# Kernel optimization log

Measured on AMD Instinct MI355X. Metric: run time of the kernel, lower is better.

Reference implementation:

```python
import jax, jax.numpy as jnp
import numpy as np

N, E, F_IN, F_E, G = 40000, 640000, 64, 16, 1000
H = F_IN * 4          # 256, GeneralConv out
O = 128               # GATv2 out (heads=1)
NEG_SLOPE = 0.2


def _glorot(key, shape):
    fan_in, fan_out = shape[0], shape[-1]
    s = jnp.sqrt(6.0 / (fan_in + fan_out))
    return jax.random.uniform(key, shape, jnp.float32, -s, s)


def setup_inputs() -> dict:
    key = jax.random.key(0)
    ks = jax.random.split(key, 20)
    x = jax.random.normal(ks[0], (N, F_IN), jnp.float32)
    edge_index = jax.random.randint(ks[1], (2, E), 0, N, jnp.int64)
    edge_attr = jax.random.normal(ks[2], (E, F_E), jnp.float32)
    batch = jnp.sort(jax.random.randint(ks[3], (N,), 0, G, jnp.int64))
    return {
        "x": x, "edge_index": edge_index, "edge_attr": edge_attr, "batch": batch,
        # GeneralConv params
        "W_msg": _glorot(ks[4], (F_IN, H)), "b_msg": jnp.zeros((H,), jnp.float32),
        "W_edge1": _glorot(ks[5], (F_E, H)), "b_edge1": jnp.zeros((H,), jnp.float32),
        "W_self": _glorot(ks[6], (F_IN, H)), "b_self": jnp.zeros((H,), jnp.float32),
        # GATv2 params (heads=1)
        "W_l": _glorot(ks[7], (H, O)), "b_l": jnp.zeros((O,), jnp.float32),
        "W_r": _glorot(ks[8], (H, O)), "b_r": jnp.zeros((O,), jnp.float32),
        "W_e2": _glorot(ks[9], (F_E, O)),
        "att": _glorot(ks[10], (O, 1))[:, 0],
        "bias2": jnp.zeros((O,), jnp.float32),
        # FFN
        "W1": _glorot(ks[11], (O, 4 * O)), "b1": jnp.zeros((4 * O,), jnp.float32),
        "W2": _glorot(ks[12], (4 * O, 1)), "b2": jnp.zeros((1,), jnp.float32),
    }


def _forward(x, edge_attr, W_msg, b_msg, W_edge1, b_edge1, W_self, b_self,
             W_l, b_l, W_r, b_r, W_e2, att, bias2, W1, b1, W2, b2,
             edge_index, batch):
    src, dst = edge_index[0], edge_index[1]
    # --- GeneralConv: msg = lin_msg(x_j) + lin_edge(edge_attr), sum-aggr at dst, + lin_self(x)
    msg = (x[src] @ W_msg + b_msg) + (edge_attr @ W_edge1 + b_edge1)  # [E,H]
    h = jax.ops.segment_sum(msg, dst, num_segments=N) + (x @ W_self + b_self)
    h = jax.nn.gelu(h, approximate=True)
    # --- GATv2Conv with self-loops (fill_value='mean' for self-loop edge_attr)
    deg = jax.ops.segment_sum(jnp.ones((E,), jnp.float32), dst, num_segments=N)
    loop_attr = jax.ops.segment_sum(edge_attr, dst, num_segments=N) / jnp.maximum(deg, 1.0)[:, None]
    nodes = jnp.arange(N, dtype=src.dtype)
    s = jnp.concatenate([src, nodes])            # [E+N]
    d = jnp.concatenate([dst, nodes])
    ea = jnp.concatenate([edge_attr, loop_attr], axis=0)
    xl = h @ W_l + b_l                           # source transform [N,O]
    xr = h @ W_r + b_r                           # target transform [N,O]
    m = xl[s] + xr[d] + ea @ W_e2                # [E+N,O]
    m = jax.nn.leaky_relu(m, NEG_SLOPE)
    alpha = m @ att                              # [E+N]
    amax = jax.ops.segment_max(alpha, d, num_segments=N)
    ea_exp = jnp.exp(alpha - amax[d])
    denom = jax.ops.segment_sum(ea_exp, d, num_segments=N)
    alpha = ea_exp / denom[d]
    out = jax.ops.segment_sum(xl[s] * alpha[:, None], d, num_segments=N) + bias2  # [N,O]
    # --- global mean pool by graph id
    cnt = jax.ops.segment_sum(jnp.ones((N,), jnp.float32), batch, num_segments=G)
    g = jax.ops.segment_sum(out, batch, num_segments=G) / jnp.maximum(cnt, 1.0)[:, None]
    # --- FFN
    y = jax.nn.gelu(g @ W1 + b1, approximate=True) @ W2 + b2  # [G,1]
    return y


def reference(x, edge_index, edge_attr, batch, W_msg, b_msg, W_edge1, b_edge1,
              W_self, b_self, W_l, b_l, W_r, b_r, W_e2, att, bias2,
              W1, b1, W2, b2):
    return _forward(x, edge_attr, W_msg, b_msg, W_edge1, b_edge1, W_self, b_self,
                    W_l, b_l, W_r, b_r, W_e2, att, bias2, W1, b1, W2, b2,
                    edge_index, batch)
```

## Files before the change

kernel.cpp:

```cpp
#include <hip/hip_runtime.h>
#include <hip/hip_bf16.h>

#define NN 40000
#define NE 640000
#define NG 1000

typedef __attribute__((ext_vector_type(8))) short short8;
typedef __attribute__((ext_vector_type(4))) float f32x4;
typedef __attribute__((ext_vector_type(2))) __bf16 bf16x2v;

__device__ __forceinline__ float gelu_t(float x) {
    float u = 0.7978845608028654f * (x + 0.044715f * x * x * x);
    return 0.5f * x * (1.0f + tanhf(u));
}
__device__ __forceinline__ void atomAddF(float* p, float v) {
    unsafeAtomicAdd(p, v);
}
__device__ __forceinline__ int rfl(int v) { return __builtin_amdgcn_readfirstlane(v); }
__device__ __forceinline__ unsigned short f2bf(float f) {
    unsigned u = __float_as_uint(f);
    unsigned r = (u + 0x7fffu + ((u >> 16) & 1u)) >> 16;
    return (unsigned short)r;
}
__device__ __forceinline__ unsigned pk_bf(float lo, float hi) {
    __hip_bfloat162 v = __float22bfloat162_rn(make_float2(lo, hi));
    unsigned r;
    __builtin_memcpy(&r, &v, 4);
    return r;
}
__device__ __forceinline__ float bfl(unsigned p) { return __uint_as_float(p << 16); }
__device__ __forceinline__ float bfh(unsigned p) { return __uint_as_float(p & 0xffff0000u); }

__device__ __forceinline__ float dot2bf(unsigned a, unsigned b, float c) {
#if __has_builtin(__builtin_amdgcn_fdot2_f32_bf16)
    bf16x2v av, bv;
    __builtin_memcpy(&av, &a, 4);
    __builtin_memcpy(&bv, &b, 4);
    return __builtin_amdgcn_fdot2_f32_bf16(av, bv, c, false);
#else
    return c + bfl(a) * bfl(b) + bfh(a) * bfh(b);
#endif
}

__global__ __launch_bounds__(256) void k_pre(
    const float* __restrict__ x, const int* __restrict__ dst,
    const float* __restrict__ W_self, const float* __restrict__ W_msg,
    const float* __restrict__ W_e1, const float* __restrict__ b_msg,
    const float* __restrict__ b_e1,
    const float* __restrict__ W_l, const float* __restrict__ W_r,
    const float* __restrict__ W_e2,
    unsigned short* __restrict__ x_bf, int* __restrict__ hist,
    int* __restrict__ rank,
    unsigned short* __restrict__ wf1, unsigned short* __restrict__ wf2,
    unsigned* __restrict__ we2p, float* __restrict__ bsum2) {
    int t = blockIdx.x * 256 + threadIdx.x;
    float4 v = ((const float4*)x)[t];
    ((uint2*)x_bf)[t] = make_uint2(pk_bf(v.x, v.y), pk_bf(v.z, v.w));
    rank[t] = atomicAdd(&hist[dst[t]], 1);
    if (t < 256) bsum2[t] = b_msg[t] + b_e1[t];
    if (t < 5120) {
        int l = t & 63;
        int kt = (t >> 6) % 5;
        int gnt = t / 320;
        int n = gnt * 16 + (l & 15);
        int k0 = kt * 32 + (l >> 4) * 8;
        unsigned short vv[8];
        #pragma unroll
        for (int j = 0; j < 8; ++j) {
            int k = k0 + j;
            float wv;
            if (k < 64)       wv = W_self[(size_t)k * 256 + n];
            else if (k < 128) wv = W_msg[(size_t)(k - 64) * 256 + n];
            else if (k < 144) wv = W_e1[(size_t)(k - 128) * 256 + n];
            else              wv = 0.f;
            vv[j] = f2bf(wv);
        }
        uint4 pack;
        pack.x = (unsigned)vv[0] | ((unsigned)vv[1] << 16);
        pack.y = (unsigned)vv[2] | ((unsigned)vv[3] << 16);
        pack.z = (unsigned)vv[4] | ((unsigned)vv[5] << 16);
        pack.w = (unsigned)vv[6] | ((unsigned)vv[7] << 16);
        ((uint4*)wf1)[t] = pack;
    }
    if (t >= 5120 && t < 13312) {
        int t2 = t - 5120;
        int l = t2 & 63;
        int kt = (t2 >> 6) & 7;
        int gnt = t2 >> 9;
        int n = gnt * 16 + (l & 15);
        int k0 = kt * 32 + (l >> 4) * 8;
        const float* W = (n < 128) ? W_l : W_r;
        int nn = n & 127;
        float w[8];
        #pragma unroll
        for (int j = 0; j < 8; ++j) w[j] = W[(size_t)(k0 + j) * 128 + nn];
        uint4 pack;
        pack.x = pk_bf(w[0], w[1]);
        pack.y = pk_bf(w[2], w[3]);
        pack.z = pk_bf(w[4], w[5]);
        pack.w = pk_bf(w[6], w[7]);
        ((uint4*)wf2)[t2] = pack;
    }
    if (t >= 13312 && t < 14336) {
        int t3 = t - 13312;
        int tt = t3 >> 7;
        int c = t3 & 127;
        we2p[t3] = pk_bf(W_e2[(size_t)(2 * tt) * 128 + c],
                         W_e2[(size_t)(2 * tt + 1) * 128 + c]);
    }
}

__global__ __launch_bounds__(1024) void k_scan(const int* __restrict__ hist,
                                               int* __restrict__ row_ptr) {
    __shared__ int ssum[1024];
    int t = threadIdx.x;
    int base = t * 40;
    int local[40];
    int s = 0;
    #pragma unroll
    for (int j = 0; j < 40; ++j) {
        int idx = base + j;
        int v = (idx < NN) ? hist[idx] : 0;
        local[j] = s;
        s += v;
    }
    ssum[t] = s;
    __syncthreads();
    for (int off = 1; off < 1024; off <<= 1) {
        int tmp = (t >= off) ? ssum[t - off] : 0;
        __syncthreads();
        ssum[t] += tmp;
        __syncthreads();
    }
    int prefix = (t > 0) ? ssum[t - 1] : 0;
    #pragma unroll
    for (int j = 0; j < 40; ++j) {
        int idx = base + j;
        if (idx < NN) row_ptr[idx] = prefix + local[j];
    }
    if (t == 0) row_ptr[NN] = NE;
}

__global__ __launch_bounds__(256) void k_scatter(const int* __restrict__ src,
                                                 const int* __restrict__ dst,
                                                 const int* __restrict__ rank,
                                                 const int* __restrict__ row_ptr,
                                                 const float* __restrict__ eattr,
                                                 int* __restrict__ csr_src,
                                                 unsigned short* __restrict__ ea_csr) {
    int e = blockIdx.x * 256 + threadIdx.x;
    if (e >= NE) return;
    int d = dst[e];
    int pos = row_ptr[d] + rank[e];
    csr_src[pos] = src[e];
    const float4* ep = (const float4*)(eattr + (size_t)e * 16);
    float4 a = ep[0], b = ep[1], c = ep[2], dd = ep[3];
    uint4 q0, q1;
    q0.x = pk_bf(a.x, a.y); q0.y = pk_bf(a.z, a.w);
    q0.z = pk_bf(b.x, b.y); q0.w = pk_bf(b.z, b.w);
    q1.x = pk_bf(c.x, c.y); q1.y = pk_bf(c.z, c.w);
    q1.z = pk_bf(dd.x, dd.y); q1.w = pk_bf(dd.z, dd.w);
    uint4* out = (uint4*)ea_csr;
    out[(size_t)pos * 2]     = q0;
    out[(size_t)pos * 2 + 1] = q1;
}

__global__ __launch_bounds__(256) void k_agg(
    const unsigned short* __restrict__ x_bf, const unsigned short* __restrict__ ea_csr,
    const int* __restrict__ csr_src, const int* __restrict__ row_ptr,
    unsigned short* __restrict__ aggx_bf, unsigned short* __restrict__ aggea_bf,
    float* __restrict__ degf) {
    int d = rfl(blockIdx.x * 4 + (threadIdx.x >> 6));
    int lane = threadIdx.x & 63;
    if (d >= NN) return;
    int beg = row_ptr[d], end = row_ptr[d + 1];
    const unsigned* xw = (const unsigned*)x_bf;
    const unsigned* eaw = (const unsigned*)ea_csr;
    int h = lane >> 5;
    int c2 = lane & 31;
    float sxa0 = 0.f, sxa1 = 0.f, sxb0 = 0.f, sxb1 = 0.f;
    int i = beg + h;
    for (; i + 2 < end; i += 4) {
        int sA = csr_src[i];
        int sB = csr_src[i + 2];
        unsigned wA = xw[(size_t)sA * 32 + c2];
        unsigned wB = xw[(size_t)sB * 32 + c2];
        sxa0 += bfl(wA); sxa1 += bfh(wA);
        sxb0 += bfl(wB); sxb1 += bfh(wB);
    }
    if (i < end) {
        int s = csr_src[i];
        unsigned w = xw[(size_t)s * 32 + c2];
        sxa0 += bfl(w); sxa1 += bfh(w);
    }
    float sx0 = sxa0 + sxb0, sx1 = sxa1 + sxb1;
    sx0 += __shfl_xor(sx0, 32, 64);
    sx1 += __shfl_xor(sx1, 32, 64);
    float se0 = 0.f, se1 = 0.f, se0b = 0.f, se1b = 0.f;
    int p = beg * 8 + lane;
    int pend = end * 8;
    for (; p + 64 < pend; p += 128) {
        unsigned w = eaw[p];
        unsigned w2 = eaw[p + 64];
        se0 += bfl(w); se1 += bfh(w);
        se0b += bfl(w2); se1b += bfh(w2);
    }
    if (p < pend) {
        unsigned w = eaw[p];
        se0 += bfl(w); se1 += bfh(w);
    }
    se0 += se0b; se1 += se1b;
    #pragma unroll
    for (int off = 8; off < 64; off <<= 1) {
        se0 += __shfl_xor(se0, off, 64);
        se1 += __shfl_xor(se1, off, 64);
    }
    if (h == 0) ((unsigned*)aggx_bf)[(size_t)d * 32 + c2] = pk_bf(sx0, sx1);
    if (lane < 8) ((unsigned*)aggea_bf)[(size_t)d * 8 + lane] = pk_bf(se0, se1);
    if (lane == 0) degf[d] = (float)(end - beg);
}

__global__ __launch_bounds__(256) void k_hx(
    const unsigned short* __restrict__ x_bf, const unsigned short* __restrict__ aggx_bf,
    const unsigned short* __restrict__ aggea_bf, const float* __restrict__ degf,
    const unsigned short* __restrict__ wf1, const unsigned short* __restrict__ wf2,
    const float* __restrict__ b_self, const float* __restrict__ bsum2,
    const float* __restrict__ b_l, const float* __restrict__ b_r,
    unsigned short* __restrict__ xl_bf, unsigned short* __restrict__ xr_bf) {
    __shared__ unsigned short hs[64][264];
    int w = threadIdx.x >> 6;
    int l = threadIdx.x & 63;
    int m0 = blockIdx.x * 64;
    int quad = l >> 4, lm = l & 15;
    {
        f32x4 acc[4][4] = {};
        short8 z8 = {0, 0, 0, 0, 0, 0, 0, 0};
        #pragma unroll
        for (int kt = 0; kt < 5; ++kt) {
            short8 a[4], b[4];
            #pragma unroll
            for (int mt = 0; mt < 4; ++mt) {
                int row = m0 + mt * 16 + lm;
                if (kt < 2)
                    a[mt] = *(const short8*)(x_bf + (size_t)row * 64 + kt * 32 + quad * 8);
                else if (kt < 4)
                    a[mt] = *(const short8*)(aggx_bf + (size_t)row * 64 + (kt - 2) * 32 + quad * 8);
                else
                    a[mt] = (quad < 2)
                        ? *(const short8*)(aggea_bf + (size_t)row * 16 + quad * 8)
                        : z8;
            }
            #pragma unroll
            for (int nt = 0; nt < 4; ++nt)
                b[nt] = *(const short8*)(wf1 + (((size_t)(w * 4 + nt) * 5 + kt) * 64 + l) * 8);
            #pragma unroll
            for (int mt = 0; mt < 4; ++mt)
                #pragma unroll
                for (int nt = 0; nt < 4; ++nt)
                    acc[mt][nt] = __builtin_amdgcn_mfma_f32_16x16x32_bf16(a[mt], b[nt], acc[mt][nt], 0, 0, 0);
        }
        #pragma unroll
        for (int nt = 0; nt < 4; ++nt) {
            int col = w * 64 + nt * 16 + lm;
            float bs = b_self[col];
            float b2 = bsum2[col];
            #pragma unroll
            for (int mt = 0; mt < 4; ++mt) {
                float4 dg = *(const float4*)(degf + m0 + mt * 16 + quad * 4);
                #pragma unroll
                for (int r = 0; r < 4; ++r) {
                    float v = gelu_t(acc[mt][nt][r] + bs + (&dg.x)[r] * b2);
                    hs[mt * 16 + quad * 4 + r][col] = f2bf(v);
                }
            }
        }
    }
    __syncthreads();
    f32x4 acc2[4][4] = {};
    #pragma unroll
    for (int kt = 0; kt < 8; ++kt) {
        short8 a[4], b[4];
        #pragma unroll
        for (int mt = 0; mt < 4; ++mt)
            a[mt] = *(const short8*)(&hs[mt * 16 + lm][kt * 32 + quad * 8]);
        #pragma unroll
        for (int nt = 0; nt < 4; ++nt)
            b[nt] = *(const short8*)(wf2 + (((size_t)(w * 4 + nt) * 8 + kt) * 64 + l) * 8);
        #pragma unroll
        for (int mt = 0; mt < 4; ++mt)
            #pragma unroll
            for (int nt = 0; nt < 4; ++nt)
                acc2[mt][nt] = __builtin_amdgcn_mfma_f32_16x16x32_bf16(a[mt], b[nt], acc2[mt][nt], 0, 0, 0);
    }
    bool isl = (w < 2);
    unsigned short* outp = isl ? xl_bf : xr_bf;
    int colbase = isl ? w * 64 : (w - 2) * 64;
    const float* bias = isl ? b_l : b_r;
    #pragma unroll
    for (int nt = 0; nt < 4; ++nt) {
        int col = colbase + nt * 16 + lm;
        float bv = bias[col];
        #pragma unroll
        for (int mt = 0; mt < 4; ++mt) {
            #pragma unroll
            for (int r = 0; r < 4; ++r) {
                int row = m0 + mt * 16 + quad * 4 + r;
                outp[(size_t)row * 128 + col] = f2bf(acc2[mt][nt][r] + bv);
            }
        }
    }
}

__device__ __forceinline__ float edge_score_pk(const unsigned* ep8,
                                               unsigned pl, float xr0, float xr1,
                                               const unsigned* wp0, const unsigned* wp1,
                                               float a0, float a1) {
    float m0 = bfl(pl) + xr0;
    float m1 = bfh(pl) + xr1;
    #pragma unroll
    for (int t = 0; t < 8; ++t) {
        m0 = dot2bf(ep8[t], wp0[t], m0);
        m1 = dot2bf(ep8[t], wp1[t], m1);
    }
    m0 = (m0 > 0.f) ? m0 : 0.2f * m0;
    m1 = (m1 > 0.f) ? m1 : 0.2f * m1;
    float part = m0 * a0 + m1 * a1;
    #pragma unroll
    for (int off = 32; off; off >>= 1) part += __shfl_xor(part, off, 64);
    return part;
}

__device__ __forceinline__ void online_upd(float al, unsigned p, float& m_run,
                                           float& l_run, float& n0, float& n1) {
    if (al > m_run) {
        float sc = __expf(m_run - al);
        l_run *= sc; n0 *= sc; n1 *= sc;
        m_run = al;
    }
    float wgt = __expf(al - m_run);
    l_run += wgt;
    n0 += wgt * bfl(p);
    n1 += wgt * bfh(p);
}

__global__ __launch_bounds__(256) void k_gat(
    const unsigned* __restrict__ xlw, const unsigned* __restrict__ xrw,
    const unsigned short* __restrict__ ea_csr, const int* __restrict__ csr_src,
    const int* __restrict__ row_ptr, const unsigned short* __restrict__ aggea_bf,
    const unsigned* __restrict__ we2p, const float* __restrict__ att,
    const float* __restrict__ bias2, const int* __restrict__ batch,
    float* __restrict__ gsum, float* __restrict__ cnt) {
    int d = rfl(blockIdx.x * 4 + (threadIdx.x >> 6));
    int lane = threadIdx.x & 63;
    if (d >= NN) return;
    unsigned wp0[8], wp1[8];
    #pragma unroll
    for (int t = 0; t < 8; ++t) {
        uint2 wv = *(const uint2*)(we2p + t * 128 + 2 * lane);
        wp0[t] = wv.x; wp1[t] = wv.y;
    }
    float2 av = *(const float2*)(att + 2 * lane);
    float a0 = av.x, a1 = av.y;
    int beg = row_ptr[d], end = row_ptr[d + 1];
    const uint4* eap = (const uint4*)ea_csr;
    unsigned pld = xlw[(size_t)d * 64 + lane];
    unsigned prd = xrw[(size_t)d * 64 + lane];
    float xr0 = bfl(prd), xr1 = bfh(prd);
    float inv = 1.0f / fmaxf((float)(end - beg), 1.0f);
    float al_loop;
    {
        const uint4* ae = (const uint4*)(aggea_bf + (size_t)d * 16);
        uint4 q0 = ae[0], q1 = ae[1];
        unsigned ep8[8] = {q0.x, q0.y, q0.z, q0.w, q1.x, q1.y, q1.z, q1.w};
        float d0 = 0.f, d1 = 0.f;
        #pragma unroll
        for (int t = 0; t < 8; ++t) {
            d0 = dot2bf(ep8[t], wp0[t], d0);
            d1 = dot2bf(ep8[t], wp1[t], d1);
        }
        float m0 = bfl(pld) + xr0 + inv * d0;
        float m1 = bfh(pld) + xr1 + inv * d1;
        m0 = (m0 > 0.f) ? m0 : 0.2f * m0;
        m1 = (m1 > 0.f) ? m1 : 0.2f * m1;
        float part = m0 * a0 + m1 * a1;
        #pragma unroll
        for (int off = 32; off; off >>= 1) part += __shfl_xor(part, off, 64);
        al_loop = part;
    }
    float m_run = al_loop, l_run = 1.0f;
    float n0 = bfl(pld), n1 = bfh(pld);
    int i = beg;
    for (; i + 3 < end; i += 4) {
        int s0 = rfl(csr_src[i]),     s1 = rfl(csr_src[i + 1]);
        int s2 = rfl(csr_src[i + 2]), s3 = rfl(csr_src[i + 3]);
        uint4 qa0 = eap[(size_t)i * 2],       qa1 = eap[(size_t)i * 2 + 1];
        uint4 qb0 = eap[(size_t)(i + 1) * 2], qb1 = eap[(size_t)(i + 1) * 2 + 1];
        uint4 qc0 = eap[(size_t)(i + 2) * 2], qc1 = eap[(size_t)(i + 2) * 2 + 1];
        uint4 qd0 = eap[(size_t)(i + 3) * 2], qd1 = eap[(size_t)(i + 3) * 2 + 1];
        unsigned p0 = xlw[(size_t)s0 * 64 + lane];
        unsigned p1 = xlw[(size_t)s1 * 64 + lane];
        unsigned p2 = xlw[(size_t)s2 * 64 + lane];
        unsigned p3 = xlw[(size_t)s3 * 64 + lane];
        unsigned e0[8] = {qa0.x, qa0.y, qa0.z, qa0.w, qa1.x, qa1.y, qa1.z, qa1.w};
        unsigned e1[8] = {qb0.x, qb0.y, qb0.z, qb0.w, qb1.x, qb1.y, qb1.z, qb1.w};
        unsigned e2[8] = {qc0.x, qc0.y, qc0.z, qc0.w, qc1.x, qc1.y, qc1.z, qc1.w};
        unsigned e3[8] = {qd0.x, qd0.y, qd0.z, qd0.w, qd1.x, qd1.y, qd1.z, qd1.w};
        float al0 = edge_score_pk(e0, p0, xr0, xr1, wp0, wp1, a0, a1);
        float al1 = edge_score_pk(e1, p1, xr0, xr1, wp0, wp1, a0, a1);
        float al2 = edge_score_pk(e2, p2, xr0, xr1, wp0, wp1, a0, a1);
        float al3 = edge_score_pk(e3, p3, xr0, xr1, wp0, wp1, a0, a1);
        float gm = fmaxf(fmaxf(al0, al1), fmaxf(al2, al3));
        if (gm > m_run) {
            float sc = __expf(m_run - gm);
            l_run *= sc; n0 *= sc; n1 *= sc;
            m_run = gm;
        }
        float w0 = __expf(al0 - m_run);
        float w1 = __expf(al1 - m_run);
        float w2 = __expf(al2 - m_run);
        float w3 = __expf(al3 - m_run);
        l_run += (w0 + w1) + (w2 + w3);
        n0 += w0 * bfl(p0) + w1 * bfl(p1) + w2 * bfl(p2) + w3 * bfl(p3);
        n1 += w0 * bfh(p0) + w1 * bfh(p1) + w2 * bfh(p2) + w3 * bfh(p3);
    }
    for (; i < end; ++i) {
        int s = rfl(csr_src[i]);
        uint4 q0 = eap[(size_t)i * 2], q1 = eap[(size_t)i * 2 + 1];
        unsigned p = xlw[(size_t)s * 64 + lane];
        unsigned e8[8] = {q0.x, q0.y, q0.z, q0.w, q1.x, q1.y, q1.z, q1.w};
        float al = edge_score_pk(e8, p, xr0, xr1, wp0, wp1, a0, a1);
        online_upd(al, p, m_run, l_run, n0, n1);
    }
    float rinv = 1.0f / l_run;
    float2 bv = *(const float2*)(bias2 + 2 * lane);
    float o0 = n0 * rinv + bv.x;
    float o1 = n1 * rinv + bv.y;
    int g = batch[d];
    atomAddF(&gsum[(size_t)g * 128 + 2 * lane], o0);
    atomAddF(&gsum[(size_t)g * 128 + 2 * lane + 1], o1);
    if (lane == 0) atomAddF(&cnt[g], 1.0f);
}

__global__ __launch_bounds__(256) void k_ffn(
    const float* __restrict__ gsum, const float* __restrict__ cnt,
    const float* __restrict__ W1, const float* __restrict__ b1,
    const float* __restrict__ W2, const float* __restrict__ b2,
    float* __restrict__ y) {
    __shared__ float row[128];
    __shared__ float red[4];
    int g = blockIdx.x;
    int t = threadIdx.x;
    if (t < 128) row[t] = gsum[(size_t)g * 128 + t] / fmaxf(cnt[g], 1.0f);
    __syncthreads();
    float part = 0.f;
    #pragma unroll
    for (int jj = 0; jj < 2; ++jj) {
        int j = t + jj * 256;
        float acc = b1[j];
        for (int k = 0; k < 128; ++k) acc += row[k] * W1[k * 512 + j];
        part += gelu_t(acc) * W2[j];
    }
    #pragma unroll
    for (int off = 32; off; off >>= 1) part += __shfl_xor(part, off, 64);
    if ((t & 63) == 0) red[t >> 6] = part;
    __syncthreads();
    if (t == 0) y[g] = red[0] + red[1] + red[2] + red[3] + b2[0];
}

extern "C" void kernel_launch(void* const* d_in, const int* in_sizes, int n_in,
                              void* d_out, int out_size, void* d_ws, size_t ws_size,
                              hipStream_t stream) {
    const float* x      = (const float*)d_in[0];
    const int*   eidx   = (const int*)d_in[1];
    const float* eattr  = (const float*)d_in[2];
    const int*   batch  = (const int*)d_in[3];
    const float* W_msg  = (const float*)d_in[4];
    const float* b_msg  = (const float*)d_in[5];
    const float* W_e1   = (const float*)d_in[6];
    const float* b_e1   = (const float*)d_in[7];
    const float* W_self = (const float*)d_in[8];
    const float* b_self = (const float*)d_in[9];
    const float* W_l    = (const float*)d_in[10];
    const float* b_l    = (const float*)d_in[11];
    const float* W_r    = (const float*)d_in[12];
    const float* b_r    = (const float*)d_in[13];
    const float* W_e2   = (const float*)d_in[14];
    const float* att    = (const float*)d_in[15];
    const float* bias2  = (const float*)d_in[16];
    const float* W1     = (const float*)d_in[17];
    const float* b1     = (const float*)d_in[18];
    const float* W2     = (const float*)d_in[19];
    const float* b2     = (const float*)d_in[20];
    const int* src = eidx;
    const int* dst = eidx + NE;

    char* wsb = (char*)d_ws;
    size_t o = 0;
    int*   hist   = (int*)(wsb + o);   o += (size_t)NN * 4;
    float* gsum   = (float*)(wsb + o); o += (size_t)NG * 128 * 4;
    float* cnt    = (float*)(wsb + o); o += 4096;
    size_t zero_bytes = o;
    int*   row_ptr = (int*)(wsb + o);  o += (size_t)(NN + 4) * 4;
    int*   rank    = (int*)(wsb + o);  o += (size_t)NE * 4;
    int*   csr_src = (int*)(wsb + o);  o += (size_t)NE * 4;
    unsigned short* ea_csr = (unsigned short*)(wsb + o); o += (size_t)NE * 16 * 2;
    unsigned short* aggx_bf  = (unsigned short*)(wsb + o); o += (size_t)NN * 64 * 2;
    unsigned short* aggea_bf = (unsigned short*)(wsb + o); o += (size_t)NN * 16 * 2;
    float* degf    = (float*)(wsb + o); o += (size_t)NN * 4;
    unsigned short* x_bf  = (unsigned short*)(wsb + o); o += (size_t)NN * 64 * 2;
    unsigned short* xl_bf = (unsigned short*)(wsb + o); o += (size_t)NN * 128 * 2;
    unsigned short* xr_bf = (unsigned short*)(wsb + o); o += (size_t)NN * 128 * 2;
    unsigned short* wf1   = (unsigned short*)(wsb + o); o += (size_t)5120 * 8 * 2;
    unsigned short* wf2   = (unsigned short*)(wsb + o); o += (size_t)8192 * 8 * 2;
    unsigned* we2p = (unsigned*)(wsb + o); o += (size_t)1024 * 4;
    float* bsum2  = (float*)(wsb + o); o += 1024;

    hipMemsetAsync(d_ws, 0, zero_bytes, stream);
    hipLaunchKernelGGL(k_pre, dim3(2500), dim3(256), 0, stream,
                       x, dst, W_self, W_msg, W_e1, b_msg, b_e1, W_l, W_r, W_e2,
                       x_bf, hist, rank, wf1, wf2, we2p, bsum2);
    hipLaunchKernelGGL(k_scan, dim3(1), dim3(1024), 0, stream, hist, row_ptr);
    hipLaunchKernelGGL(k_scatter, dim3(2500), dim3(256), 0, stream,
                       src, dst, rank, row_ptr, eattr, csr_src, ea_csr);
    hipLaunchKernelGGL(k_agg, dim3((NN + 3) / 4), dim3(256), 0, stream,
                       x_bf, ea_csr, csr_src, row_ptr, aggx_bf, aggea_bf, degf);
    hipLaunchKernelGGL(k_hx, dim3(625), dim3(256), 0, stream,
                       x_bf, aggx_bf, aggea_bf, degf, wf1, wf2,
                       b_self, bsum2, b_l, b_r, xl_bf, xr_bf);
    hipLaunchKernelGGL(k_gat, dim3((NN + 3) / 4), dim3(256), 0, stream,
                       (const unsigned*)xl_bf, (const unsigned*)xr_bf, ea_csr,
                       csr_src, row_ptr, aggea_bf, we2p, att, bias2,
                       batch, gsum, cnt);
    hipLaunchKernelGGL(k_ffn, dim3(NG), dim3(256), 0, stream,
                       gsum, cnt, W1, b1, W2, b2, (float*)d_out);
}
```

Before: 383.8 us.

## Partition degree histogram by edge chunk and split GAT edges across half-waves

The degree histogram is split into 8 partitions, one per 80000-edge chunk, to reduce atomic contention, and the scan now reduces over partitions and emits per-partition offsets used by the scatter. The GAT kernel has each half-wavefront handle a different edge, with every lane covering 4 output columns, so one wave scores two edges per step. The halves' softmax accumulators are combined at the end with a cross-half shuffle. This trades an 8x larger histogram and a heavier single-block scan for fewer contended atomics and shorter shuffle reductions in the GAT loop.

After: 947.3 us. +146.8%, slower.

```diff
diff --git a/kernel.cpp b/kernel.cpp
--- a/kernel.cpp
+++ b/kernel.cpp
@@ -56,7 +56,8 @@
     int t = blockIdx.x * 256 + threadIdx.x;
     float4 v = ((const float4*)x)[t];
     ((uint2*)x_bf)[t] = make_uint2(pk_bf(v.x, v.y), pk_bf(v.z, v.w));
-    rank[t] = atomicAdd(&hist[dst[t]], 1);
+    int part = t / 80000;
+    rank[t] = atomicAdd(&hist[part * NN + dst[t]], 1);
     if (t < 256) bsum2[t] = b_msg[t] + b_e1[t];
     if (t < 5120) {
         int l = t & 63;
@@ -111,32 +112,46 @@
 }
 
 __global__ __launch_bounds__(1024) void k_scan(const int* __restrict__ hist,
-                                               int* __restrict__ row_ptr) {
+                                               int* __restrict__ row_ptr,
+                                               int* __restrict__ off) {
     __shared__ int ssum[1024];
     int t = threadIdx.x;
     int base = t * 40;
-    int local[40];
+    int locpre[40];
     int s = 0;
-    #pragma unroll
+    #pragma unroll 4
     for (int j = 0; j < 40; ++j) {
         int idx = base + j;
-        int v = (idx < NN) ? hist[idx] : 0;
-        local[j] = s;
-        s += v;
+        int dsum = 0;
+        if (idx < NN) {
+            #pragma unroll
+            for (int p = 0; p < 8; ++p) dsum += hist[p * NN + idx];
+        }
+        locpre[j] = s;
+        s += dsum;
     }
     ssum[t] = s;
     __syncthreads();
-    for (int off = 1; off < 1024; off <<= 1) {
-        int tmp = (t >= off) ? ssum[t - off] : 0;
+    for (int o = 1; o < 1024; o <<= 1) {
+        int tmp = (t >= o) ? ssum[t - o] : 0;
         __syncthreads();
         ssum[t] += tmp;
         __syncthreads();
     }
     int prefix = (t > 0) ? ssum[t - 1] : 0;
-    #pragma unroll
+    #pragma unroll 4
     for (int j = 0; j < 40; ++j) {
         int idx = base + j;
-        if (idx < NN) row_ptr[idx] = prefix + local[j];
+        if (idx < NN) {
+            int start = prefix + locpre[j];
+            row_ptr[idx] = start;
+            int acc = start;
+            #pragma unroll
+            for (int p = 0; p < 8; ++p) {
+                off[p * NN + idx] = acc;
+                acc += hist[p * NN + idx];
+            }
+        }
     }
     if (t == 0) row_ptr[NN] = NE;
 }
@@ -144,14 +159,15 @@
 __global__ __launch_bounds__(256) void k_scatter(const int* __restrict__ src,
                                                  const int* __restrict__ dst,
                                                  const int* __restrict__ rank,
-                                                 const int* __restrict__ row_ptr,
+                                                 const int* __restrict__ off,
                                                  const float* __restrict__ eattr,
                                                  int* __restrict__ csr_src,
                                                  unsigned short* __restrict__ ea_csr) {
     int e = blockIdx.x * 256 + threadIdx.x;
     if (e >= NE) return;
     int d = dst[e];
-    int pos = row_ptr[d] + rank[e];
+    int p = e / 80000;
+    int pos = off[p * NN + d] + rank[e];
     csr_src[pos] = src[e];
     const float4* ep = (const float4*)(eattr + (size_t)e * 16);
     float4 a = ep[0], b = ep[1], c = ep[2], dd = ep[3];
@@ -311,36 +327,31 @@
     }
 }
 
-__device__ __forceinline__ float edge_score_pk(const unsigned* ep8,
-                                               unsigned pl, float xr0, float xr1,
-                                               const unsigned* wp0, const unsigned* wp1,
-                                               float a0, float a1) {
-    float m0 = bfl(pl) + xr0;
-    float m1 = bfh(pl) + xr1;
+__device__ __forceinline__ float score4(uint4 q0, uint4 q1, uint2 pl,
+                                        float xr0, float xr1, float xr2, float xr3,
+                                        const unsigned* w0, const unsigned* w1,
+                                        const unsigned* w2, const unsigned* w3,
+                                        float4 av) {
+    unsigned ep8[8] = {q0.x, q0.y, q0.z, q0.w, q1.x, q1.y, q1.z, q1.w};
+    float m0 = bfl(pl.x) + xr0;
+    float m1 = bfh(pl.x) + xr1;
+    float m2 = bfl(pl.y) + xr2;
+    float m3 = bfh(pl.y) + xr3;
     #pragma unroll
     for (int t = 0; t < 8; ++t) {
-        m0 = dot2bf(ep8[t], wp0[t], m0);
-        m1 = dot2bf(ep8[t], wp1[t], m1);
+        m0 = dot2bf(ep8[t], w0[t], m0);
+        m1 = dot2bf(ep8[t], w1[t], m1);
+        m2 = dot2bf(ep8[t], w2[t], m2);
+        m3 = dot2bf(ep8[t], w3[t], m3);
     }
     m0 = (m0 > 0.f) ? m0 : 0.2f * m0;
     m1 = (m1 > 0.f) ? m1 : 0.2f * m1;
-    float part = m0 * a0 + m1 * a1;
-    #pragma unroll
-    for (int off = 32; off; off >>= 1) part += __shfl_xor(part, off, 64);
+    m2 = (m2 > 0.f) ? m2 : 0.2f * m2;
+    m3 = (m3 > 0.f) ? m3 : 0.2f * m3;
+    float part = (m0 * av.x + m1 * av.y) + (m2 * av.z + m3 * av.w);
+    #pragma unroll
+    for (int off = 1; off <= 16; off <<= 1) part += __shfl_xor(part, off, 64);
     return part;
-}
-
-__device__ __forceinline__ void online_upd(float al, unsigned p, float& m_run,
-                                           float& l_run, float& n0, float& n1) {
-    if (al > m_run) {
-        float sc = __expf(m_run - al);
-        l_run *= sc; n0 *= sc; n1 *= sc;
-        m_run = al;
-    }
-    float wgt = __expf(al - m_run);
-    l_run += wgt;
-    n0 += wgt * bfl(p);
-    n1 += wgt * bfh(p);
 }
 
 __global__ __launch_bounds__(256) void k_gat(
@@ -353,92 +364,128 @@
     int d = rfl(blockIdx.x * 4 + (threadIdx.x >> 6));
     int lane = threadIdx.x & 63;
     if (d >= NN) return;
-    unsigned wp0[8], wp1[8];
+    int hl = lane & 31;
+    int half = lane >> 5;
+    unsigned w0[8], w1[8], w2[8], w3[8];
     #pragma unroll
     for (int t = 0; t < 8; ++t) {
-        uint2 wv = *(const uint2*)(we2p + t * 128 + 2 * lane);
-        wp0[t] = wv.x; wp1[t] = wv.y;
-    }
-    float2 av = *(const float2*)(att + 2 * lane);
-    float a0 = av.x, a1 = av.y;
+        uint4 wv = *(const uint4*)(we2p + t * 128 + 4 * hl);
+        w0[t] = wv.x; w1[t] = wv.y; w2[t] = wv.z; w3[t] = wv.w;
+    }
+    float4 av = *(const float4*)(att + 4 * hl);
     int beg = row_ptr[d], end = row_ptr[d + 1];
     const uint4* eap = (const uint4*)ea_csr;
-    unsigned pld = xlw[(size_t)d * 64 + lane];
-    unsigned prd = xrw[(size_t)d * 64 + lane];
-    float xr0 = bfl(prd), xr1 = bfh(prd);
+    uint2 prd = *(const uint2*)(xrw + (size_t)d * 64 + 2 * hl);
+    uint2 pld = *(const uint2*)(xlw + (size_t)d * 64 + 2 * hl);
+    float xr0 = bfl(prd.x), xr1 = bfh(prd.x), xr2 = bfl(prd.y), xr3 = bfh(prd.y);
     float inv = 1.0f / fmaxf((float)(end - beg), 1.0f);
     float al_loop;
     {
         const uint4* ae = (const uint4*)(aggea_bf + (size_t)d * 16);
         uint4 q0 = ae[0], q1 = ae[1];
         unsigned ep8[8] = {q0.x, q0.y, q0.z, q0.w, q1.x, q1.y, q1.z, q1.w};
-        float d0 = 0.f, d1 = 0.f;
+        float d0 = 0.f, d1 = 0.f, d2 = 0.f, d3 = 0.f;
         #pragma unroll
         for (int t = 0; t < 8; ++t) {
-            d0 = dot2bf(ep8[t], wp0[t], d0);
-            d1 = dot2bf(ep8[t], wp1[t], d1);
-        }
-        float m0 = bfl(pld) + xr0 + inv * d0;
-        float m1 = bfh(pld) + xr1 + inv * d1;
+            d0 = dot2bf(ep8[t], w0[t], d0);
+            d1 = dot2bf(ep8[t], w1[t], d1);
+            d2 = dot2bf(ep8[t], w2[t], d2);
+            d3 = dot2bf(ep8[t], w3[t], d3);
+        }
+        float m0 = bfl(pld.x) + xr0 + inv * d0;
+        float m1 = bfh(pld.x) + xr1 + inv * d1;
+        float m2 = bfl(pld.y) + xr2 + inv * d2;
+        float m3 = bfh(pld.y) + xr3 + inv * d3;
         m0 = (m0 > 0.f) ? m0 : 0.2f * m0;
         m1 = (m1 > 0.f) ? m1 : 0.2f * m1;
-        float part = m0 * a0 + m1 * a1;
-        #pragma unroll
-        for (int off = 32; off; off >>= 1) part += __shfl_xor(part, off, 64);
+        m2 = (m2 > 0.f) ? m2 : 0.2f * m2;
+        m3 = (m3 > 0.f) ? m3 : 0.2f * m3;
+        float part = (m0 * av.x + m1 * av.y) + (m2 * av.z + m3 * av.w);
+        #pragma unroll
+        for (int off = 1; off <= 16; off <<= 1) part += __shfl_xor(part, off, 64);
         al_loop = part;
     }
-    float m_run = al_loop, l_run = 1.0f;
-    float n0 = bfl(pld), n1 = bfh(pld);
+    float m_run = m_run = al_loop;
+    float l_run = (half == 0) ? 1.0f : 0.0f;
+    float n0 = (half == 0) ? bfl(pld.x) : 0.f;
+    float n1 = (half == 0) ? bfh(pld.x) : 0.f;
+    float n2 = (half == 0) ? bfl(pld.y) : 0.f;
+    float n3 = (half == 0) ? bfh(pld.y) : 0.f;
     int i = beg;
     for (; i + 3 < end; i += 4) {
-        int s0 = rfl(csr_src[i]),     s1 = rfl(csr_src[i + 1]);
-        int s2 = rfl(csr_src[i + 2]), s3 = rfl(csr_src[i + 3]);
-        uint4 qa0 = eap[(size_t)i * 2],       qa1 = eap[(size_t)i * 2 + 1];
-        uint4 qb0 = eap[(size_t)(i + 1) * 2], qb1 = eap[(size_t)(i + 1) * 2 + 1];
-        uint4 qc0 = eap[(size_t)(i + 2) * 2], qc1 = eap[(size_t)(i + 2) * 2 + 1];
-        uint4 qd0 = eap[(size_t)(i + 3) * 2], qd1 = eap[(size_t)(i + 3) * 2 + 1];
-        unsigned p0 = xlw[(size_t)s0 * 64 + lane];
-        unsigned p1 = xlw[(size_t)s1 * 64 + lane];
-        unsigned p2 = xlw[(size_t)s2 * 64 + lane];
-        unsigned p3 = xlw[(size_t)s3 * 64 + lane];
-        unsigned e0[8] = {qa0.x, qa0.y, qa0.z, qa0.w, qa1.x, qa1.y, qa1.z, qa1.w};
-        unsigned e1[8] = {qb0.x, qb0.y, qb0.z, qb0.w, qb1.x, qb1.y, qb1.z, qb1.w};
-        unsigned e2[8] = {qc0.x, qc0.y, qc0.z, qc0.w, qc1.x, qc1.y, qc1.z, qc1.w};
-        unsigned e3[8] = {qd0.x, qd0.y, qd0.z, qd0.w, qd1.x, qd1.y, qd1.z, qd1.w};
-        float al0 = edge_score_pk(e0, p0, xr0, xr1, wp0, wp1, a0, a1);
-        float al1 = edge_score_pk(e1, p1, xr0, xr1, wp0, wp1, a0, a1);
-        float al2 = edge_score_pk(e2, p2, xr0, xr1, wp0, wp1, a0, a1);
-        float al3 = edge_score_pk(e3, p3, xr0, xr1, wp0, wp1, a0, a1);
+        int ia = i + half;
+        int ib = i + 2 + half;
+        int sa = csr_src[ia];
+        int sb = csr_src[ib];
+        uint2 pa = *(const uint2*)(xlw + (size_t)sa * 64 + 2 * hl);
+        uint2 pb = *(const uint2*)(xlw + (size_t)sb * 64 + 2 * hl);
+        uint4 qa0 = eap[(size_t)ia * 2], qa1 = eap[(size_t)ia * 2 + 1];
+        uint4 qb0 = eap[(size_t)ib * 2], qb1 = eap[(size_t)ib * 2 + 1];
+        float partA = score4(qa0, qa1, pa, xr0, xr1, xr2, xr3, w0, w1, w2, w3, av);
+        float partB = score4(qb0, qb1, pb, xr0, xr1, xr2, xr3, w0, w1, w2, w3, av);
+        float al0 = __shfl(partA, 0, 64);
+        float al1 = __shfl(partA, 32, 64);
+        float al2 = __shfl(partB, 0, 64);
+        float al3 = __shfl(partB, 32, 64);
         float gm = fmaxf(fmaxf(al0, al1), fmaxf(al2, al3));
         if (gm > m_run) {
             float sc = __expf(m_run - gm);
-            l_run *= sc; n0 *= sc; n1 *= sc;
+            l_run *= sc; n0 *= sc; n1 *= sc; n2 *= sc; n3 *= sc;
             m_run = gm;
         }
-        float w0 = __expf(al0 - m_run);
-        float w1 = __expf(al1 - m_run);
-        float w2 = __expf(al2 - m_run);
-        float w3 = __expf(al3 - m_run);
-        l_run += (w0 + w1) + (w2 + w3);
-        n0 += w0 * bfl(p0) + w1 * bfl(p1) + w2 * bfl(p2) + w3 * bfl(p3);
-        n1 += w0 * bfh(p0) + w1 * bfh(p1) + w2 * bfh(p2) + w3 * bfh(p3);
-    }
-    for (; i < end; ++i) {
-        int s = rfl(csr_src[i]);
-        uint4 q0 = eap[(size_t)i * 2], q1 = eap[(size_t)i * 2 + 1];
-        unsigned p = xlw[(size_t)s * 64 + lane];
-        unsigned e8[8] = {q0.x, q0.y, q0.z, q0.w, q1.x, q1.y, q1.z, q1.w};
-        float al = edge_score_pk(e8, p, xr0, xr1, wp0, wp1, a0, a1);
-        online_upd(al, p, m_run, l_run, n0, n1);
-    }
-    float rinv = 1.0f / l_run;
-    float2 bv = *(const float2*)(bias2 + 2 * lane);
-    float o0 = n0 * rinv + bv.x;
-    float o1 = n1 * rinv + bv.y;
-    int g = batch[d];
-    atomAddF(&gsum[(size_t)g * 128 + 2 * lane], o0);
-    atomAddF(&gsum[(size_t)g * 128 + 2 * lane + 1], o1);
-    if (lane == 0) atomAddF(&cnt[g], 1.0f);
+        float e0 = __expf(al0 - m_run);
+        float e1 = __expf(al1 - m_run);
+        float e2 = __expf(al2 - m_run);
+        float e3 = __expf(al3 - m_run);
+        float wa = half ? e1 : e0;
+        float wb = half ? e3 : e2;
+        l_run += wa + wb;
+        n0 += wa * bfl(pa.x) + wb * bfl(pb.x);
+        n1 += wa * bfh(pa.x) + wb * bfh(pb.x);
+        n2 += wa * bfl(pa.y) + wb * bfl(pb.y);
+        n3 += wa * bfh(pa.y) + wb * bfh(pb.y);
+    }
+    for (; i < end; i += 2) {
+        int ie = i + half;
+        bool vmine = ie < end;
+        int idx = vmine ? ie : (end - 1);
+        int s = csr_src[idx];
+        uint2 p = *(const uint2*)(xlw + (size_t)s * 64 + 2 * hl);
+        uint4 q0 = eap[(size_t)idx * 2], q1 = eap[(size_t)idx * 2 + 1];
+        float part = score4(q0, q1, p, xr0, xr1, xr2, xr3, w0, w1, w2, w3, av);
+        float alA = __shfl(part, 0, 64);
+        float alB = __shfl(part, 32, 64);
+        bool vB = (i + 1) < end;
+        float gm = vB ? fmaxf(alA, alB) : alA;
+        if (gm > m_run) {
+            float sc = __expf(m_run - gm);
+            l_run *= sc; n0 *= sc; n1 *= sc; n2 *= sc; n3 *= sc;
+            m_run = gm;
+        }
+        float eA = __expf(alA - m_run);
+        float eB = vB ? __expf(alB - m_run) : 0.f;
+        float wme = half ? eB : eA;
+        l_run += wme;
+        n0 += wme * bfl(p.x);
+        n1 += wme * bfh(p.x);
+        n2 += wme * bfl(p.y);
+        n3 += wme * bfh(p.y);
+    }
+    l_run += __shfl_xor(l_run, 32, 64);
+    n0 += __shfl_xor(n0, 32, 64);
+    n1 += __shfl_xor(n1, 32, 64);
+    n2 += __shfl_xor(n2, 32, 64);
+    n3 += __shfl_xor(n3, 32, 64);
+    if (half == 0) {
+        float rinv = 1.0f / l_run;
+        float4 bv = *(const float4*)(bias2 + 4 * hl);
+        int g = batch[d];
+        atomAddF(&gsum[(size_t)g * 128 + 4 * hl + 0], n0 * rinv + bv.x);
+        atomAddF(&gsum[(size_t)g * 128 + 4 * hl + 1], n1 * rinv + bv.y);
+        atomAddF(&gsum[(size_t)g * 128 + 4 * hl + 2], n2 * rinv + bv.z);
+        atomAddF(&gsum[(size_t)g * 128 + 4 * hl + 3], n3 * rinv + bv.w);
+        if (hl == 0) atomAddF(&cnt[g], 1.0f);
+    }
 }
 
 __global__ __launch_bounds__(256) void k_ffn(
@@ -496,11 +543,12 @@
 
     char* wsb = (char*)d_ws;
     size_t o = 0;
-    int*   hist   = (int*)(wsb + o);   o += (size_t)NN * 4;
+    int*   hist   = (int*)(wsb + o);   o += (size_t)8 * NN * 4;
     float* gsum   = (float*)(wsb + o); o += (size_t)NG * 128 * 4;
     float* cnt    = (float*)(wsb + o); o += 4096;
     size_t zero_bytes = o;
     int*   row_ptr = (int*)(wsb + o);  o += (size_t)(NN + 4) * 4;
+    int*   off     = (int*)(wsb + o);  o += (size_t)8 * NN * 4;
     int*   rank    = (int*)(wsb + o);  o += (size_t)NE * 4;
     int*   csr_src = (int*)(wsb + o);  o += (size_t)NE * 4;
     unsigned short* ea_csr = (unsigned short*)(wsb + o); o += (size_t)NE * 16 * 2;
@@ -519,9 +567,9 @@
     hipLaunchKernelGGL(k_pre, dim3(2500), dim3(256), 0, stream,
                        x, dst, W_self, W_msg, W_e1, b_msg, b_e1, W_l, W_r, W_e2,
                        x_bf, hist, rank, wf1, wf2, we2p, bsum2);
-    hipLaunchKernelGGL(k_scan, dim3(1), dim3(1024), 0, stream, hist, row_ptr);
+    hipLaunchKernelGGL(k_scan, dim3(1), dim3(1024), 0, stream, hist, row_ptr, off);
     hipLaunchKernelGGL(k_scatter, dim3(2500), dim3(256), 0, stream,
-                       src, dst, rank, row_ptr, eattr, csr_src, ea_csr);
+                       src, dst, rank, off, eattr, csr_src, ea_csr);
     hipLaunchKernelGGL(k_agg, dim3((NN + 3) / 4), dim3(256), 0, stream,
                        x_bf, ea_csr, csr_src, row_ptr, aggx_bf, aggea_bf, degf);
     hipLaunchKernelGGL(k_hx, dim3(625), dim3(256), 0, stream,
```

## Partition degree histogram into eight slices to reduce atomic contention

Applied to the files above, without the earlier changes.

The destination histogram used for CSR construction is split into eight per-edge-range partitions, so atomics collide less. New kernels sum the partitions, scan the totals (now with vectorized int4 loads and stores), and compute per-partition offsets that the scatter uses. This adds two kernel launches, a larger memset and extra histogram traffic in exchange for lower atomic contention.

Measured after the change: 369.9 us. 3.6% less time.

```diff
diff --git a/kernel.cpp b/kernel.cpp
--- a/kernel.cpp
+++ b/kernel.cpp
@@ -56,7 +56,8 @@
     int t = blockIdx.x * 256 + threadIdx.x;
     float4 v = ((const float4*)x)[t];
     ((uint2*)x_bf)[t] = make_uint2(pk_bf(v.x, v.y), pk_bf(v.z, v.w));
-    rank[t] = atomicAdd(&hist[dst[t]], 1);
+    int part = t / 80000;
+    rank[t] = atomicAdd(&hist[part * NN + dst[t]], 1);
     if (t < 256) bsum2[t] = b_msg[t] + b_e1[t];
     if (t < 5120) {
         int l = t & 63;
@@ -110,48 +111,80 @@
     }
 }
 
-__global__ __launch_bounds__(1024) void k_scan(const int* __restrict__ hist,
+__global__ __launch_bounds__(256) void k_dsum(const int* __restrict__ hist,
+                                              int* __restrict__ dsum) {
+    int idx = blockIdx.x * 256 + threadIdx.x;
+    if (idx >= 40960) return;
+    int s = 0;
+    if (idx < NN) {
+        #pragma unroll
+        for (int p = 0; p < 8; ++p) s += hist[p * NN + idx];
+    }
+    dsum[idx] = s;
+}
+
+__global__ __launch_bounds__(1024) void k_scan(const int* __restrict__ dsum,
                                                int* __restrict__ row_ptr) {
     __shared__ int ssum[1024];
     int t = threadIdx.x;
     int base = t * 40;
+    const int4* dv = (const int4*)(dsum + base);
     int local[40];
     int s = 0;
     #pragma unroll
-    for (int j = 0; j < 40; ++j) {
-        int idx = base + j;
-        int v = (idx < NN) ? hist[idx] : 0;
-        local[j] = s;
-        s += v;
+    for (int j = 0; j < 10; ++j) {
+        int4 v = dv[j];
+        local[j * 4 + 0] = s; s += v.x;
+        local[j * 4 + 1] = s; s += v.y;
+        local[j * 4 + 2] = s; s += v.z;
+        local[j * 4 + 3] = s; s += v.w;
     }
     ssum[t] = s;
     __syncthreads();
-    for (int off = 1; off < 1024; off <<= 1) {
-        int tmp = (t >= off) ? ssum[t - off] : 0;
+    for (int o = 1; o < 1024; o <<= 1) {
+        int tmp = (t >= o) ? ssum[t - o] : 0;
         __syncthreads();
         ssum[t] += tmp;
         __syncthreads();
     }
     int prefix = (t > 0) ? ssum[t - 1] : 0;
-    #pragma unroll
-    for (int j = 0; j < 40; ++j) {
-        int idx = base + j;
-        if (idx < NN) row_ptr[idx] = prefix + local[j];
-    }
-    if (t == 0) row_ptr[NN] = NE;
+    int4* rv = (int4*)(row_ptr + base);
+    #pragma unroll
+    for (int j = 0; j < 10; ++j) {
+        int4 o4;
+        o4.x = prefix + local[j * 4 + 0];
+        o4.y = prefix + local[j * 4 + 1];
+        o4.z = prefix + local[j * 4 + 2];
+        o4.w = prefix + local[j * 4 + 3];
+        rv[j] = o4;
+    }
+}
+
+__global__ __launch_bounds__(256) void k_off(const int* __restrict__ hist,
+                                             const int* __restrict__ row_ptr,
+                                             int* __restrict__ off) {
+    int idx = blockIdx.x * 256 + threadIdx.x;
+    if (idx >= NN) return;
+    int acc = row_ptr[idx];
+    #pragma unroll
+    for (int p = 0; p < 8; ++p) {
+        off[p * NN + idx] = acc;
+        acc += hist[p * NN + idx];
+    }
 }
 
 __global__ __launch_bounds__(256) void k_scatter(const int* __restrict__ src,
                                                  const int* __restrict__ dst,
                                                  const int* __restrict__ rank,
-                                                 const int* __restrict__ row_ptr,
+                                                 const int* __restrict__ off,
                                                  const float* __restrict__ eattr,
                                                  int* __restrict__ csr_src,
                                                  unsigned short* __restrict__ ea_csr) {
     int e = blockIdx.x * 256 + threadIdx.x;
     if (e >= NE) return;
     int d = dst[e];
-    int pos = row_ptr[d] + rank[e];
+    int p = e / 80000;
+    int pos = off[p * NN + d] + rank[e];
     csr_src[pos] = src[e];
     const float4* ep = (const float4*)(eattr + (size_t)e * 16);
     float4 a = ep[0], b = ep[1], c = ep[2], dd = ep[3];
@@ -496,11 +529,13 @@
 
     char* wsb = (char*)d_ws;
     size_t o = 0;
-    int*   hist   = (int*)(wsb + o);   o += (size_t)NN * 4;
+    int*   hist   = (int*)(wsb + o);   o += (size_t)8 * NN * 4;
     float* gsum   = (float*)(wsb + o); o += (size_t)NG * 128 * 4;
     float* cnt    = (float*)(wsb + o); o += 4096;
     size_t zero_bytes = o;
-    int*   row_ptr = (int*)(wsb + o);  o += (size_t)(NN + 4) * 4;
+    int*   dsum    = (int*)(wsb + o);  o += (size_t)40960 * 4;
+    int*   row_ptr = (int*)(wsb + o);  o += (size_t)40964 * 4;
+    int*   off     = (int*)(wsb + o);  o += (size_t)8 * NN * 4;
     int*   rank    = (int*)(wsb + o);  o += (size_t)NE * 4;
     int*   csr_src = (int*)(wsb + o);  o += (size_t)NE * 4;
     unsigned short* ea_csr = (unsigned short*)(wsb + o); o += (size_t)NE * 16 * 2;
@@ -519,9 +554,12 @@
     hipLaunchKernelGGL(k_pre, dim3(2500), dim3(256), 0, stream,
                        x, dst, W_self, W_msg, W_e1, b_msg, b_e1, W_l, W_r, W_e2,
                        x_bf, hist, rank, wf1, wf2, we2p, bsum2);
-    hipLaunchKernelGGL(k_scan, dim3(1), dim3(1024), 0, stream, hist, row_ptr);
+    hipLaunchKernelGGL(k_dsum, dim3(160), dim3(256), 0, stream, hist, dsum);
+    hipLaunchKernelGGL(k_scan, dim3(1), dim3(1024), 0, stream, dsum, row_ptr);
+    hipLaunchKernelGGL(k_off, dim3((NN + 255) / 256), dim3(256), 0, stream,
+                       hist, row_ptr, off);
     hipLaunchKernelGGL(k_scatter, dim3(2500), dim3(256), 0, stream,
-                       src, dst, rank, row_ptr, eattr, csr_src, ea_csr);
+                       src, dst, rank, off, eattr, csr_src, ea_csr);
     hipLaunchKernelGGL(k_agg, dim3((NN + 3) / 4), dim3(256), 0, stream,
                        x_bf, ea_csr, csr_src, row_ptr, aggx_bf, aggea_bf, degf);
     hipLaunchKernelGGL(k_hx, dim3(625), dim3(256), 0, stream,
```
